# Kernel tuning notes

Hardware: AMD Instinct MI355X
Metric: run time of the kernel (lower is better)

The kernel has to match this reference:

```python
import jax, jax.numpy as jnp
import numpy as np

D_MODEL = 512
N_HEADS = 8
D_HEAD = D_MODEL // N_HEADS
N_LAYERS = 6
VOCAB = 32000
B, S = 4, 1024
EPS = 1e-5


def positional_encoding(length, d_model):
    # matches get_positional_encoding_table: pos * (1/10000**(i/d)), sin on even i, cos on odd i
    inv = 1.0 / (10000.0 ** (jnp.arange(d_model, dtype=jnp.float32) / d_model))
    ang = jnp.arange(length, dtype=jnp.float32)[:, None] * inv[None, :]  # [S, D]
    pe = jnp.where(jnp.arange(d_model) % 2 == 0, jnp.sin(ang), jnp.cos(ang))
    return pe


def layer_norm(x, g, b):
    m = jnp.mean(x, axis=-1, keepdims=True)
    v = jnp.mean((x - m) ** 2, axis=-1, keepdims=True)
    return (x - m) * jax.lax.rsqrt(v + EPS) * g + b


def setup_inputs() -> dict:
    key = jax.random.key(0)
    ks = jax.random.split(key, 9)
    sc = 0.02
    return {
        "tokens": jax.random.randint(ks[0], (B, S), 0, VOCAB),
        "emb": jax.random.normal(ks[1], (VOCAB, D_MODEL), jnp.float32) * sc,
        "Wq": jax.random.normal(ks[2], (N_LAYERS, D_MODEL, D_MODEL), jnp.float32) * sc,
        "bq": jnp.zeros((N_LAYERS, D_MODEL), jnp.float32),
        "Wk": jax.random.normal(ks[3], (N_LAYERS, D_MODEL, D_MODEL), jnp.float32) * sc,
        "bk": jnp.zeros((N_LAYERS, D_MODEL), jnp.float32),
        "Wv": jax.random.normal(ks[4], (N_LAYERS, D_MODEL, D_MODEL), jnp.float32) * sc,
        "bv": jnp.zeros((N_LAYERS, D_MODEL), jnp.float32),
        "Wo": jax.random.normal(ks[5], (N_LAYERS, D_MODEL, D_MODEL), jnp.float32) * sc,
        "bo": jnp.zeros((N_LAYERS, D_MODEL), jnp.float32),
        "W1": jax.random.normal(ks[6], (N_LAYERS, D_MODEL, 4 * D_MODEL), jnp.float32) * sc,
        "b1": jnp.zeros((N_LAYERS, 4 * D_MODEL), jnp.float32),
        "W2": jax.random.normal(ks[7], (N_LAYERS, 4 * D_MODEL, D_MODEL), jnp.float32) * sc,
        "b2": jnp.zeros((N_LAYERS, D_MODEL), jnp.float32),
        "ln_g": jnp.ones((N_LAYERS, D_MODEL), jnp.float32),
        "ln_b": jnp.zeros((N_LAYERS, D_MODEL), jnp.float32),
    }


def encoder_layer(x, Wq, bq, Wk, bk, Wv, bv, Wo, bo, W1, b1, W2, b2, g, b):
    bsz = x.shape[0]
    q = (x @ Wq + bq).reshape(bsz, -1, N_HEADS, D_HEAD).transpose(0, 2, 1, 3)  # [B,h,S,dk]
    k = (x @ Wk + bk).reshape(bsz, -1, N_HEADS, D_HEAD).transpose(0, 2, 1, 3)
    v = (x @ Wv + bv).reshape(bsz, -1, N_HEADS, D_HEAD).transpose(0, 2, 1, 3)
    scores = jnp.einsum('bhqd,bhkd->bhqk', q, k) / (D_HEAD ** 0.5)
    w = jax.nn.softmax(scores, axis=-1)
    attn = jnp.einsum('bhqk,bhkd->bhqd', w, v)  # [B,h,S,dv]
    # faithful to source bug: .view(B,-1,h*dv) WITHOUT transposing heads back
    attn = attn.reshape(bsz, -1, N_HEADS * D_HEAD)  # [B,S,D] with heads/seq interleaved
    x = layer_norm(x + (attn @ Wo + bo), g, b)
    ffn = jnp.maximum(x @ W1 + b1, 0.0) @ W2 + b2
    x = layer_norm(x + ffn, g, b)  # same (shared) LayerNorm params, as in source
    return x


def reference(tokens, emb, Wq, bq, Wk, bk, Wv, bv, Wo, bo, W1, b1, W2, b2, ln_g, ln_b):
    x = emb[tokens]  # [B,S,D]
    x = x + positional_encoding(x.shape[1], D_MODEL)
    for i in range(N_LAYERS):
        x = encoder_layer(x, Wq[i], bq[i], Wk[i], bk[i], Wv[i], bv[i], Wo[i], bo[i],
                          W1[i], b1[i], W2[i], b2[i], ln_g[i], ln_b[i])
    return x
```

## Files before the change

kernel.cpp:

```cpp
#include <hip/hip_runtime.h>
#include <hip/hip_bf16.h>
#include <math.h>

typedef unsigned short ushort_t;
typedef __attribute__((ext_vector_type(8))) short bfrag_t;
typedef __attribute__((ext_vector_type(4))) float facc_t;

#define D_MODEL 512
#define NH 8
#define DH 64
#define NL 6
#define BB 4
#define SS 1024
#define ROWS (BB*SS)
#define DFF 2048

__device__ inline ushort_t f2bf(float f) {
    __hip_bfloat16 h = __float2bfloat16(f);
    return *(ushort_t*)&h;
}
__device__ inline void gload_lds16(const void* g, void* l) {
    __builtin_amdgcn_global_load_lds((const __attribute__((address_space(1))) unsigned int*)g,
                                     (__attribute__((address_space(3))) unsigned int*)l, 16, 0, 0);
}

__global__ __launch_bounds__(256) void embed_pe(const int* __restrict__ tok,
                                                const float* __restrict__ emb,
                                                float* __restrict__ x,
                                                ushort_t* __restrict__ xbf) {
    int row = blockIdx.x;
    int s = row & (SS - 1);
    int t = tok[row];
    const float* e = emb + (size_t)t * D_MODEL;
    for (int i = threadIdx.x; i < D_MODEL; i += 256) {
        float freq = __expf(-9.210340371976184f * ((float)i / (float)D_MODEL));
        float ang = (float)s * freq;
        float pe = (i & 1) ? cosf(ang) : sinf(ang);
        float v = e[i] + pe;
        x[(size_t)row * D_MODEL + i] = v;
        xbf[(size_t)row * D_MODEL + i] = f2bf(v);
    }
}

__global__ __launch_bounds__(256) void prep_weights(const float* __restrict__ Wq,
                                                    const float* __restrict__ Wk,
                                                    const float* __restrict__ Wv,
                                                    const float* __restrict__ Wo,
                                                    const float* __restrict__ W1,
                                                    const float* __restrict__ W2,
                                                    int layer, ushort_t* __restrict__ wlay) {
    __shared__ float tile[32][33];
    int z = blockIdx.z;
    const float* src; ushort_t* dst; int K, N;
    size_t o512 = (size_t)layer * 512 * 512;
    size_t o1M  = (size_t)layer * 512 * 2048;
    switch (z) {
        case 0: src = Wq + o512; dst = wlay;               K = 512;  N = 512;  break;
        case 1: src = Wk + o512; dst = wlay + 262144;      K = 512;  N = 512;  break;
        case 2: src = Wv + o512; dst = wlay + 524288;      K = 512;  N = 512;  break;
        case 3: src = Wo + o512; dst = wlay + 786432;      K = 512;  N = 512;  break;
        case 4: src = W1 + o1M;  dst = wlay + 1048576;     K = 512;  N = 2048; break;
        default:src = W2 + o1M;  dst = wlay + 2097152;     K = 2048; N = 512;  break;
    }
    int n0 = blockIdx.x * 32, k0 = blockIdx.y * 32;
    if (n0 >= N || k0 >= K) return;
    int tx = threadIdx.x & 31, ty = threadIdx.x >> 5;
    #pragma unroll
    for (int i = 0; i < 4; i++)
        tile[ty + i * 8][tx] = src[(size_t)(k0 + ty + i * 8) * N + n0 + tx];
    __syncthreads();
    #pragma unroll
    for (int i = 0; i < 4; i++)
        dst[(size_t)(n0 + ty + i * 8) * K + k0 + tx] = f2bf(tile[tx][ty + i * 8]);
}

__global__ __launch_bounds__(256) void concat_bias(const float* __restrict__ bq,
                                                   const float* __restrict__ bk,
                                                   const float* __restrict__ bv,
                                                   float* __restrict__ bqkv) {
    int l = blockIdx.x;
    for (int i = threadIdx.x; i < 1536; i += 256) {
        float v = (i < 512) ? bq[l * 512 + i]
                : (i < 1024) ? bk[l * 512 + i - 512]
                : bv[l * 512 + i - 1024];
        bqkv[l * 1536 + i] = v;
    }
}

__global__ __launch_bounds__(256) void gemm_mfma(const ushort_t* __restrict__ A,
                                                 const ushort_t* __restrict__ Bt,
                                                 const float* __restrict__ bias,
                                                 float* __restrict__ Cf,
                                                 ushort_t* __restrict__ Cb,
                                                 int N, int K, int relu) {
    __shared__ ushort_t lA[128 * 64];
    __shared__ ushort_t lB[128 * 64];

    const int tid = threadIdx.x;
    const int w = tid >> 6, lane = tid & 63;
    const int wr = w & 1, wc = w >> 1;
    const int lane16 = lane & 15, quad = lane >> 4;
    const int row0 = blockIdx.y * 128, col0 = blockIdx.x * 128;

    facc_t acc[4][4];
    #pragma unroll
    for (int i = 0; i < 4; i++)
        #pragma unroll
        for (int j = 0; j < 4; j++)
            acc[i][j] = (facc_t){0.f, 0.f, 0.f, 0.f};

    for (int k0 = 0; k0 < K; k0 += 64) {
        __syncthreads();
        #pragma unroll
        for (int i = 0; i < 4; i++) {
            int g = w * 256 + i * 64 + lane;
            int r = g >> 3, p = g & 7;
            int q = p ^ (r & 7);
            gload_lds16(A + (size_t)(row0 + r) * K + k0 + q * 8, lA + (size_t)g * 8);
            gload_lds16(Bt + (size_t)(col0 + r) * K + k0 + q * 8, lB + (size_t)g * 8);
        }
        __syncthreads();

        #pragma unroll
        for (int kk = 0; kk < 2; kk++) {
            bfrag_t af[4], bfg[4];
            #pragma unroll
            for (int t = 0; t < 4; t++) {
                int m = wr * 64 + t * 16 + lane16;
                int q = kk * 4 + quad;
                af[t] = *(const bfrag_t*)(lA + ((size_t)m * 8 + (q ^ (m & 7))) * 8);
                int n = wc * 64 + t * 16 + lane16;
                bfg[t] = *(const bfrag_t*)(lB + ((size_t)n * 8 + (q ^ (n & 7))) * 8);
            }
            #pragma unroll
            for (int ti = 0; ti < 4; ti++)
                #pragma unroll
                for (int tj = 0; tj < 4; tj++)
                    acc[ti][tj] = __builtin_amdgcn_mfma_f32_16x16x32_bf16(
                        af[ti], bfg[tj], acc[ti][tj], 0, 0, 0);
        }
    }

    float bv_[4];
    #pragma unroll
    for (int tj = 0; tj < 4; tj++)
        bv_[tj] = bias[col0 + wc * 64 + tj * 16 + lane16];

    #pragma unroll
    for (int ti = 0; ti < 4; ti++) {
        int grow_base = row0 + wr * 64 + ti * 16 + quad * 4;
        #pragma unroll
        for (int tj = 0; tj < 4; tj++) {
            int gcol = col0 + wc * 64 + tj * 16 + lane16;
            #pragma unroll
            for (int rr = 0; rr < 4; rr++) {
                float v = acc[ti][tj][rr] + bv_[tj];
                if (relu) v = fmaxf(v, 0.f);
                size_t idx = (size_t)(grow_base + rr) * N + gcol;
                if (Cf) Cf[idx] = v;
                if (Cb) Cb[idx] = f2bf(v);
            }
        }
    }
}

__global__ __launch_bounds__(256) void gemm_mfma64(const ushort_t* __restrict__ A,
                                                   const ushort_t* __restrict__ Bt,
                                                   const float* __restrict__ bias,
                                                   float* __restrict__ Cf,
                                                   ushort_t* __restrict__ Cb,
                                                   int N, int K, int relu) {
    __shared__ ushort_t lA[64 * 64];
    __shared__ ushort_t lB[64 * 64];

    const int tid = threadIdx.x;
    const int w = tid >> 6, lane = tid & 63;
    const int wr = w & 1, wc = w >> 1;
    const int lane16 = lane & 15, quad = lane >> 4;
    const int row0 = blockIdx.y * 64, col0 = blockIdx.x * 64;

    facc_t acc[2][2];
    #pragma unroll
    for (int i = 0; i < 2; i++)
        #pragma unroll
        for (int j = 0; j < 2; j++)
            acc[i][j] = (facc_t){0.f, 0.f, 0.f, 0.f};

    for (int k0 = 0; k0 < K; k0 += 64) {
        __syncthreads();
        #pragma unroll
        for (int i = 0; i < 2; i++) {
            int g = w * 128 + i * 64 + lane;
            int r = g >> 3, p = g & 7;
            int q = p ^ (r & 7);
            gload_lds16(A + (size_t)(row0 + r) * K + k0 + q * 8, lA + (size_t)g * 8);
            gload_lds16(Bt + (size_t)(col0 + r) * K + k0 + q * 8, lB + (size_t)g * 8);
        }
        __syncthreads();

        #pragma unroll
        for (int kk = 0; kk < 2; kk++) {
            bfrag_t af[2], bfg[2];
            #pragma unroll
            for (int t = 0; t < 2; t++) {
                int m = wr * 32 + t * 16 + lane16;
                int q = kk * 4 + quad;
                af[t] = *(const bfrag_t*)(lA + ((size_t)m * 8 + (q ^ (m & 7))) * 8);
                int n = wc * 32 + t * 16 + lane16;
                bfg[t] = *(const bfrag_t*)(lB + ((size_t)n * 8 + (q ^ (n & 7))) * 8);
            }
            #pragma unroll
            for (int ti = 0; ti < 2; ti++)
                #pragma unroll
                for (int tj = 0; tj < 2; tj++)
                    acc[ti][tj] = __builtin_amdgcn_mfma_f32_16x16x32_bf16(
                        af[ti], bfg[tj], acc[ti][tj], 0, 0, 0);
        }
    }

    float bv_[2];
    #pragma unroll
    for (int tj = 0; tj < 2; tj++)
        bv_[tj] = bias[col0 + wc * 32 + tj * 16 + lane16];

    #pragma unroll
    for (int ti = 0; ti < 2; ti++) {
        int grow_base = row0 + wr * 32 + ti * 16 + quad * 4;
        #pragma unroll
        for (int tj = 0; tj < 2; tj++) {
            int gcol = col0 + wc * 32 + tj * 16 + lane16;
            #pragma unroll
            for (int rr = 0; rr < 4; rr++) {
                float v = acc[ti][tj][rr] + bv_[tj];
                if (relu) v = fmaxf(v, 0.f);
                size_t idx = (size_t)(grow_base + rr) * N + gcol;
                if (Cf) Cf[idx] = v;
                if (Cb) Cb[idx] = f2bf(v);
            }
        }
    }
}

__global__ __launch_bounds__(128) void attn_mfma(const ushort_t* __restrict__ qkv,
                                                 ushort_t* __restrict__ ab) {
    __shared__ __align__(16) ushort_t lK[2][4096];
    __shared__ __align__(16) ushort_t lVT[2][4096];
    __shared__ __align__(16) ushort_t lP[2048];

    const int tid = threadIdx.x;
    const int w = tid >> 6, lane = tid & 63;
    const int lane16 = lane & 15, quad = lane >> 4;
    const int qt = blockIdx.x, h = blockIdx.y, b = blockIdx.z;

    const ushort_t* Qrow = qkv + (size_t)(b * SS + qt * 32 + w * 16 + lane16) * 1536 + h * 64;
    bfrag_t qa[2];
    #pragma unroll
    for (int ks = 0; ks < 2; ks++)
        qa[ks] = *(const bfrag_t*)(Qrow + ks * 32 + quad * 8);

    facc_t O[4];
    #pragma unroll
    for (int t = 0; t < 4; t++) O[t] = (facc_t){0.f, 0.f, 0.f, 0.f};
    float mrow[4] = {-INFINITY, -INFINITY, -INFINITY, -INFINITY};
    float lrow[4] = {0.f, 0.f, 0.f, 0.f};

    const int vkey = tid & 63;
    const int vdg  = tid >> 6;
    const int vk8 = vkey >> 3, vj = vkey & 7;

    const float LOG2E = 1.4426950408889634f;
    const float SC = 0.125f * 1.4426950408889634f;

    auto stageK = [&](int kt, int buf) {
        #pragma unroll
        for (int i = 0; i < 4; i++) {
            int g = i * 128 + tid;
            int r = g >> 3, p = g & 7;
            int q = p ^ (r & 7);
            gload_lds16(qkv + (size_t)(b * SS + kt * 64 + r) * 1536 + h * 64 + 512 + q * 8,
                        &lK[buf][(size_t)g * 8]);
        }
    };
    auto loadV = [&](int kt, ushort_t* vs) {
        const ushort_t* vsrc = qkv + (size_t)(b * SS + kt * 64 + vkey) * 1536
                               + h * 64 + 1024 + vdg * 32;
        #pragma unroll
        for (int i4 = 0; i4 < 4; i4++)
            *(uint4*)(vs + i4 * 8) = *(const uint4*)(vsrc + i4 * 8);
    };
    auto writeV = [&](const ushort_t* vs, int buf) {
        #pragma unroll
        for (int e = 0; e < 32; e++) {
            int n = vdg * 32 + e;
            lVT[buf][(size_t)(n * 8 + (vk8 ^ (n & 7))) * 8 + vj] = vs[e];
        }
    };

    {
        ushort_t v0[32];
        stageK(0, 0);
        loadV(0, v0);
        writeV(v0, 0);
    }
    __syncthreads();

    for (int kt = 0; kt < 16; kt++) {
        const int cur = kt & 1;

        ushort_t vn[32];
        if (kt < 15) {
            stageK(kt + 1, cur ^ 1);
            loadV(kt + 1, vn);
        }

        facc_t sf[4];
        #pragma unroll
        for (int t = 0; t < 4; t++) sf[t] = (facc_t){0.f, 0.f, 0.f, 0.f};
        #pragma unroll
        for (int ks = 0; ks < 2; ks++) {
            #pragma unroll
            for (int t = 0; t < 4; t++) {
                int row = t * 16 + lane16;
                int q = ks * 4 + quad;
                bfrag_t kf = *(const bfrag_t*)(&lK[cur][((size_t)row * 8 + (q ^ (row & 7))) * 8]);
                sf[t] = __builtin_amdgcn_mfma_f32_16x16x32_bf16(qa[ks], kf, sf[t], 0, 0, 0);
            }
        }

        float mt_[4];
        #pragma unroll
        for (int r = 0; r < 4; r++)
            mt_[r] = fmaxf(fmaxf(sf[0][r], sf[1][r]), fmaxf(sf[2][r], sf[3][r])) * 0.125f;
        #pragma unroll
        for (int off = 1; off < 16; off <<= 1)
            #pragma unroll
            for (int r = 0; r < 4; r++)
                mt_[r] = fmaxf(mt_[r], __shfl_xor(mt_[r], off));

        bool small = (mt_[0] <= mrow[0] + 8.f) && (mt_[1] <= mrow[1] + 8.f)
                  && (mt_[2] <= mrow[2] + 8.f) && (mt_[3] <= mrow[3] + 8.f);
        if (!__all(small)) {
            #pragma unroll
            for (int r = 0; r < 4; r++) {
                float mn = fmaxf(mrow[r], mt_[r]);
                float al = __builtin_amdgcn_exp2f((mrow[r] - mn) * LOG2E);
                mrow[r] = mn;
                lrow[r] *= al;
                O[0][r] *= al; O[1][r] *= al; O[2][r] *= al; O[3][r] *= al;
            }
        }
        float mC[4];
        #pragma unroll
        for (int r = 0; r < 4; r++) mC[r] = mrow[r] * LOG2E;

        float ps[4] = {0.f, 0.f, 0.f, 0.f};
        ushort_t* Pw = lP + w * 1024;
        #pragma unroll
        for (int t = 0; t < 4; t++) {
            int k8 = t * 2 + (lane16 >> 3);
            int j = lane16 & 7;
            #pragma unroll
            for (int r = 0; r < 4; r++) {
                float p = __builtin_amdgcn_exp2f(fmaf(sf[t][r], SC, -mC[r]));
                ps[r] += p;
                int row = quad * 4 + r;
                Pw[(size_t)(row * 8 + (k8 ^ (row & 7))) * 8 + j] = f2bf(p);
            }
        }
        #pragma unroll
        for (int off = 1; off < 16; off <<= 1)
            #pragma unroll
            for (int r = 0; r < 4; r++)
                ps[r] += __shfl_xor(ps[r], off);
        #pragma unroll
        for (int r = 0; r < 4; r++)
            lrow[r] += ps[r];

        #pragma unroll
        for (int ks = 0; ks < 2; ks++) {
            int q = ks * 4 + quad;
            bfrag_t pf = *(const bfrag_t*)(Pw + ((size_t)lane16 * 8 + (q ^ (lane16 & 7))) * 8);
            #pragma unroll
            for (int t = 0; t < 4; t++) {
                int n = t * 16 + lane16;
                bfrag_t vf = *(const bfrag_t*)(&lVT[cur][((size_t)n * 8 + (q ^ (n & 7))) * 8]);
                O[t] = __builtin_amdgcn_mfma_f32_16x16x32_bf16(pf, vf, O[t], 0, 0, 0);
            }
        }

        if (kt < 15) writeV(vn, cur ^ 1);

        __syncthreads();
    }

    size_t obase = ((size_t)((b * NH + h) * SS) + qt * 32 + w * 16 + quad * 4) * DH;
    #pragma unroll
    for (int r = 0; r < 4; r++) {
        float inv = 1.f / lrow[r];
        #pragma unroll
        for (int t = 0; t < 4; t++)
            ab[obase + (size_t)r * DH + t * 16 + lane16] = f2bf(O[t][r] * inv);
    }
}

__global__ __launch_bounds__(256) void add_ln(const float* __restrict__ x,
                                              const float* __restrict__ delta,
                                              const float* __restrict__ g,
                                              const float* __restrict__ bparm,
                                              float* __restrict__ outf,
                                              ushort_t* __restrict__ outb) {
    __shared__ float red[2][4];
    int row = blockIdx.x;
    int t = threadIdx.x;
    const float* xr = x + (size_t)row * D_MODEL;
    const float* dr = delta + (size_t)row * D_MODEL;
    float v0 = xr[t] + dr[t];
    float v1 = xr[t + 256] + dr[t + 256];
    float s = v0 + v1;
    float ss = v0 * v0 + v1 * v1;
    #pragma unroll
    for (int off = 1; off < 64; off <<= 1) {
        s  += __shfl_xor(s, off);
        ss += __shfl_xor(ss, off);
    }
    int lane = t & 63, wid = t >> 6;
    if (lane == 0) { red[0][wid] = s; red[1][wid] = ss; }
    __syncthreads();
    s  = red[0][0] + red[0][1] + red[0][2] + red[0][3];
    ss = red[1][0] + red[1][1] + red[1][2] + red[1][3];
    float mean = s * (1.f / D_MODEL);
    float var = ss * (1.f / D_MODEL) - mean * mean;
    float rinv = rsqrtf(var + 1e-5f);
    float o0 = (v0 - mean) * rinv * g[t]       + bparm[t];
    float o1 = (v1 - mean) * rinv * g[t + 256] + bparm[t + 256];
    float* orow = outf + (size_t)row * D_MODEL;
    orow[t] = o0; orow[t + 256] = o1;
    ushort_t* brow = outb + (size_t)row * D_MODEL;
    brow[t] = f2bf(o0); brow[t + 256] = f2bf(o1);
}

extern "C" void kernel_launch(void* const* d_in, const int* in_sizes, int n_in,
                              void* d_out, int out_size, void* d_ws, size_t ws_size,
                              hipStream_t stream) {
    const int* tokens = (const int*)d_in[0];
    const float* emb = (const float*)d_in[1];
    const float* Wq = (const float*)d_in[2];  const float* bq = (const float*)d_in[3];
    const float* Wk = (const float*)d_in[4];  const float* bk = (const float*)d_in[5];
    const float* Wv = (const float*)d_in[6];  const float* bv = (const float*)d_in[7];
    const float* Wo = (const float*)d_in[8];  const float* bo = (const float*)d_in[9];
    const float* W1 = (const float*)d_in[10]; const float* b1 = (const float*)d_in[11];
    const float* W2 = (const float*)d_in[12]; const float* b2 = (const float*)d_in[13];
    const float* lng = (const float*)d_in[14]; const float* lnb = (const float*)d_in[15];

    char* base = (char*)d_ws;
    ushort_t* wlay = (ushort_t*)(base);
    float*    bqkv = (float*)   (base + 6291456);
    float*    x    = (float*)   (base + 6328320);
    ushort_t* xbf  = (ushort_t*)(base + 14716928);
    float*    tmp  = (float*)   (base + 18911232);
    ushort_t* qkv  = (ushort_t*)(base + 27299840);
    ushort_t* ab   = (ushort_t*)(base + 39882752);
    ushort_t* mid  = qkv;

    ushort_t* wqkv_t = wlay;
    ushort_t* wo_t   = wlay + 786432;
    ushort_t* w1_t   = wlay + 1048576;
    ushort_t* w2_t   = wlay + 2097152;

    concat_bias<<<NL, 256, 0, stream>>>(bq, bk, bv, bqkv);
    embed_pe<<<ROWS, 256, 0, stream>>>(tokens, emb, x, xbf);

    for (int l = 0; l < NL; l++) {
        prep_weights<<<dim3(64, 64, 6), 256, 0, stream>>>(Wq, Wk, Wv, Wo, W1, W2, l, wlay);

        gemm_mfma<<<dim3(12, 32), 256, 0, stream>>>(xbf, wqkv_t, bqkv + l * 1536,
                                                    nullptr, qkv, 1536, 512, 0);
        attn_mfma<<<dim3(32, NH, BB), 128, 0, stream>>>(qkv, ab);

        gemm_mfma64<<<dim3(8, 64), 256, 0, stream>>>(ab, wo_t, bo + l * D_MODEL,
                                                     tmp, nullptr, 512, 512, 0);
        add_ln<<<ROWS, 256, 0, stream>>>(x, tmp, lng + l * D_MODEL, lnb + l * D_MODEL,
                                         x, xbf);

        gemm_mfma<<<dim3(16, 32), 256, 0, stream>>>(xbf, w1_t, b1 + l * DFF,
                                                    nullptr, mid, 2048, 512, 1);
        gemm_mfma64<<<dim3(8, 64), 256, 0, stream>>>(mid, w2_t, b2 + l * D_MODEL,
                                                     tmp, nullptr, 512, 2048, 0);
        float* lnout = (l == NL - 1) ? (float*)d_out : x;
        add_ln<<<ROWS, 256, 0, stream>>>(x, tmp, lng + l * D_MODEL, lnb + l * D_MODEL,
                                         lnout, xbf);
    }
}
```

Measured before the change: 940.1 us.

## Split attention over key halves and merge partial results in a combine kernel

Attention now runs with the key range split into two halves per query tile, doubling the block count. Each half writes a normalized partial output plus row max and sum. A new combine kernel merges the halves with softmax rescaling. The K/V double buffering is replaced with single buffering. The change adds an extra launch and intermediate traffic, and loses load/compute overlap.

```diff
diff --git a/kernel.cpp b/kernel.cpp
--- a/kernel.cpp
+++ b/kernel.cpp
@@ -18,6 +18,11 @@
 __device__ inline ushort_t f2bf(float f) {
     __hip_bfloat16 h = __float2bfloat16(f);
     return *(ushort_t*)&h;
+}
+__device__ inline float bf2f(ushort_t u) {
+    unsigned int x = ((unsigned int)u) << 16;
+    union { unsigned int i; float f; } c; c.i = x;
+    return c.f;
 }
 __device__ inline void gload_lds16(const void* g, void* l) {
     __builtin_amdgcn_global_load_lds((const __attribute__((address_space(1))) unsigned int*)g,
@@ -241,16 +246,19 @@
     }
 }
 
-__global__ __launch_bounds__(128) void attn_mfma(const ushort_t* __restrict__ qkv,
-                                                 ushort_t* __restrict__ ab) {
-    __shared__ __align__(16) ushort_t lK[2][4096];
-    __shared__ __align__(16) ushort_t lVT[2][4096];
+__global__ __launch_bounds__(128) void attn_mfma_split(const ushort_t* __restrict__ qkv,
+                                                       ushort_t* __restrict__ Yp,
+                                                       float2* __restrict__ mlp) {
+    __shared__ __align__(16) ushort_t lK[4096];
+    __shared__ __align__(16) ushort_t lVT[4096];
     __shared__ __align__(16) ushort_t lP[2048];
 
     const int tid = threadIdx.x;
     const int w = tid >> 6, lane = tid & 63;
     const int lane16 = lane & 15, quad = lane >> 4;
-    const int qt = blockIdx.x, h = blockIdx.y, b = blockIdx.z;
+    const int qt = blockIdx.x, h = blockIdx.y;
+    const int b = blockIdx.z >> 1, kh = blockIdx.z & 1;
+    const int kt0 = kh * 8;
 
     const ushort_t* Qrow = qkv + (size_t)(b * SS + qt * 32 + w * 16 + lane16) * 1536 + h * 64;
     bfrag_t qa[2];
@@ -271,14 +279,14 @@
     const float LOG2E = 1.4426950408889634f;
     const float SC = 0.125f * 1.4426950408889634f;
 
-    auto stageK = [&](int kt, int buf) {
+    auto stageK = [&](int kt) {
         #pragma unroll
         for (int i = 0; i < 4; i++) {
             int g = i * 128 + tid;
             int r = g >> 3, p = g & 7;
             int q = p ^ (r & 7);
             gload_lds16(qkv + (size_t)(b * SS + kt * 64 + r) * 1536 + h * 64 + 512 + q * 8,
-                        &lK[buf][(size_t)g * 8]);
+                        lK + (size_t)g * 8);
         }
     };
     auto loadV = [&](int kt, ushort_t* vs) {
@@ -288,30 +296,23 @@
         for (int i4 = 0; i4 < 4; i4++)
             *(uint4*)(vs + i4 * 8) = *(const uint4*)(vsrc + i4 * 8);
     };
-    auto writeV = [&](const ushort_t* vs, int buf) {
+    auto writeV = [&](const ushort_t* vs) {
         #pragma unroll
         for (int e = 0; e < 32; e++) {
             int n = vdg * 32 + e;
-            lVT[buf][(size_t)(n * 8 + (vk8 ^ (n & 7))) * 8 + vj] = vs[e];
+            lVT[(size_t)(n * 8 + (vk8 ^ (n & 7))) * 8 + vj] = vs[e];
         }
     };
 
-    {
-        ushort_t v0[32];
-        stageK(0, 0);
-        loadV(0, v0);
-        writeV(v0, 0);
-    }
-    __syncthreads();
-
-    for (int kt = 0; kt < 16; kt++) {
-        const int cur = kt & 1;
-
-        ushort_t vn[32];
-        if (kt < 15) {
-            stageK(kt + 1, cur ^ 1);
-            loadV(kt + 1, vn);
-        }
+    ushort_t vcur[32];
+    loadV(kt0, vcur);
+
+    for (int kt = kt0; kt < kt0 + 8; kt++) {
+        stageK(kt);
+        writeV(vcur);
+        __syncthreads();
+
+        if (kt < kt0 + 7) loadV(kt + 1, vcur);
 
         facc_t sf[4];
         #pragma unroll
@@ -322,7 +323,7 @@
             for (int t = 0; t < 4; t++) {
                 int row = t * 16 + lane16;
                 int q = ks * 4 + quad;
-                bfrag_t kf = *(const bfrag_t*)(&lK[cur][((size_t)row * 8 + (q ^ (row & 7))) * 8]);
+                bfrag_t kf = *(const bfrag_t*)(lK + ((size_t)row * 8 + (q ^ (row & 7))) * 8);
                 sf[t] = __builtin_amdgcn_mfma_f32_16x16x32_bf16(qa[ks], kf, sf[t], 0, 0, 0);
             }
         }
@@ -383,24 +384,47 @@
             #pragma unroll
             for (int t = 0; t < 4; t++) {
                 int n = t * 16 + lane16;
-                bfrag_t vf = *(const bfrag_t*)(&lVT[cur][((size_t)n * 8 + (q ^ (n & 7))) * 8]);
+                bfrag_t vf = *(const bfrag_t*)(lVT + ((size_t)n * 8 + (q ^ (n & 7))) * 8);
                 O[t] = __builtin_amdgcn_mfma_f32_16x16x32_bf16(pf, vf, O[t], 0, 0, 0);
             }
         }
-
-        if (kt < 15) writeV(vn, cur ^ 1);
-
         __syncthreads();
     }
 
-    size_t obase = ((size_t)((b * NH + h) * SS) + qt * 32 + w * 16 + quad * 4) * DH;
+    size_t rbase = ((size_t)(kh * BB + b) * NH + h) * SS + qt * 32 + w * 16 + quad * 4;
     #pragma unroll
     for (int r = 0; r < 4; r++) {
         float inv = 1.f / lrow[r];
         #pragma unroll
         for (int t = 0; t < 4; t++)
-            ab[obase + (size_t)r * DH + t * 16 + lane16] = f2bf(O[t][r] * inv);
-    }
+            Yp[(rbase + r) * DH + t * 16 + lane16] = f2bf(O[t][r] * inv);
+        if (lane16 == 0)
+            mlp[rbase + r] = make_float2(mrow[r], lrow[r]);
+    }
+}
+
+__global__ __launch_bounds__(256) void attn_combine(const ushort_t* __restrict__ Yp,
+                                                    const float2* __restrict__ mlp,
+                                                    ushort_t* __restrict__ ab) {
+    const float LOG2E = 1.4426950408889634f;
+    int rid = blockIdx.x * 32 + (threadIdx.x >> 3);
+    int d0 = (threadIdx.x & 7) * 8;
+    float2 ml0 = mlp[rid];
+    float2 ml1 = mlp[32768 + rid];
+    float m = fmaxf(ml0.x, ml1.x);
+    float a0 = __builtin_amdgcn_exp2f((ml0.x - m) * LOG2E) * ml0.y;
+    float a1 = __builtin_amdgcn_exp2f((ml1.x - m) * LOG2E) * ml1.y;
+    float inv = 1.f / (a0 + a1);
+    a0 *= inv; a1 *= inv;
+    uint4 u0 = *(const uint4*)(Yp + (size_t)rid * DH + d0);
+    uint4 u1 = *(const uint4*)(Yp + (size_t)32768 * DH + (size_t)rid * DH + d0);
+    const ushort_t* p0 = (const ushort_t*)&u0;
+    const ushort_t* p1 = (const ushort_t*)&u1;
+    ushort_t o[8];
+    #pragma unroll
+    for (int e = 0; e < 8; e++)
+        o[e] = f2bf(a0 * bf2f(p0[e]) + a1 * bf2f(p1[e]));
+    *(uint4*)(ab + (size_t)rid * DH + d0) = *(uint4*)o;
 }
 
 __global__ __launch_bounds__(256) void add_ln(const float* __restrict__ x,
@@ -462,6 +486,9 @@
     ushort_t* ab   = (ushort_t*)(base + 39882752);
     ushort_t* mid  = qkv;
 
+    ushort_t* Yp  = (ushort_t*)tmp;
+    float2*   mlp = (float2*)xbf;
+
     ushort_t* wqkv_t = wlay;
     ushort_t* wo_t   = wlay + 786432;
     ushort_t* w1_t   = wlay + 1048576;
@@ -475,7 +502,8 @@
 
         gemm_mfma<<<dim3(12, 32), 256, 0, stream>>>(xbf, wqkv_t, bqkv + l * 1536,
                                                     nullptr, qkv, 1536, 512, 0);
-        attn_mfma<<<dim3(32, NH, BB), 128, 0, stream>>>(qkv, ab);
+        attn_mfma_split<<<dim3(32, NH, BB * 2), 128, 0, stream>>>(qkv, Yp, mlp);
+        attn_combine<<<1024, 256, 0, stream>>>(Yp, mlp, ab);
 
         gemm_mfma64<<<dim3(8, 64), 256, 0, stream>>>(ab, wo_t, bo + l * D_MODEL,
                                                      tmp, nullptr, 512, 512, 0);
```

Result: slower. 973.2 us (+3.5%).
